# Performance work log

Measured on AMD Instinct MI355X. Metric: run time of the kernel, lower is better.

## Reference

```python
import jax, jax.numpy as jnp
import numpy as np

NUM_EXPERT = 8
IN_FEAT = 1024
OUT_FEAT = 1024
N_TOKENS = 8192


def setup_inputs() -> dict:
    key = jax.random.key(0)
    k_inp, k_gate, k_w = jax.random.split(key, 3)
    inp = jax.random.normal(k_inp, (N_TOKENS, IN_FEAT), dtype=jnp.float32)
    gate = jax.random.randint(k_gate, (N_TOKENS,), 0, NUM_EXPERT, dtype=jnp.int32)
    # FMoELinear weight: [num_expert, out_feat, in_feat], kaiming-uniform-like init
    bound = 1.0 / np.sqrt(IN_FEAT)
    weight = jax.random.uniform(
        k_w, (NUM_EXPERT, OUT_FEAT, IN_FEAT), dtype=jnp.float32,
        minval=-bound, maxval=bound)
    return {"inp": inp, "gate": gate, "weight": weight}


def reference(inp, gate, weight):
    # out[i] = weight[gate[i]] @ inp[i]  (top-1 MoE dispatch + grouped GEMM + combine)
    # Loop over the small fixed expert set via scan; each step does a masked
    # dense GEMM so only tokens routed to expert e contribute.
    n, _ = inp.shape
    num_expert, out_feat, _ = weight.shape

    def body(acc, ew):
        e, w_e = ew  # w_e: [out_feat, in_feat]
        mask = (gate == e).astype(inp.dtype)[:, None]  # [n, 1]
        acc = acc + (inp * mask) @ w_e.T               # [n, out_feat]
        return acc, None

    init = jnp.zeros((n, out_feat), dtype=inp.dtype)
    out, _ = jax.lax.scan(body, init, (jnp.arange(num_expert), weight))
    return out
```

## Files before the change

kernel.cpp:

```cpp
#include <hip/hip_runtime.h>
#include <hip/hip_bf16.h>

#define N_TOKENS 8192
#define IN_FEAT 1024
#define OUT_FEAT 1024
#define NUM_EXPERT 8

#define BM 128
#define BN 128
#define BK 32

typedef __bf16 bf16x8 __attribute__((ext_vector_type(8)));
typedef float f32x4 __attribute__((ext_vector_type(4)));

__device__ __forceinline__ unsigned int rne16(float x) {
    union { float f; unsigned int u; } c;
    c.f = x;
    unsigned int u = c.u;
    u += 0x7fffu + ((u >> 16) & 1u);
    return u >> 16;
}
__device__ __forceinline__ unsigned int pk2(float x, float y) {
    return rne16(x) | (rne16(y) << 16);
}

__device__ __forceinline__ void load_lds16(const void* g, void* l) {
    __builtin_amdgcn_global_load_lds(
        (const __attribute__((address_space(1))) unsigned int*)g,
        (__attribute__((address_space(3))) unsigned int*)l,
        16, 0, 0);
}

__global__ __launch_bounds__(1024) void moe_setup(const int* __restrict__ gate,
                                                  int* __restrict__ seg,
                                                  int* __restrict__ cur) {
    __shared__ int lc[NUM_EXPERT];
    const int t = threadIdx.x;
    const int lane = t & 63;
    if (t < NUM_EXPERT) lc[t] = 0;
    __syncthreads();
    #pragma unroll
    for (int i = 0; i < 8; ++i) {
        int g = gate[t + i * 1024];
        #pragma unroll
        for (int e = 0; e < NUM_EXPERT; ++e) {
            unsigned long long m = __ballot(g == e);
            if (lane == 0 && m) atomicAdd(&lc[e], __popcll(m));
        }
    }
    __syncthreads();
    if (t == 0) {
        int s = 0;
        #pragma unroll
        for (int e = 0; e < NUM_EXPERT; ++e) { seg[e] = s; cur[e] = s; s += lc[e]; }
        seg[NUM_EXPERT] = s;
    }
}

__global__ __launch_bounds__(256) void moe_scatter(const int* __restrict__ gate,
                                                   int* __restrict__ cur,
                                                   int* __restrict__ perm) {
    const int t = threadIdx.x;
    const int lane = t & 63;
    const unsigned long long lt = (lane == 0) ? 0ull : (~0ull >> (64 - lane));
    const int i = blockIdx.x * 256 + t;
    int g = gate[i];
    #pragma unroll
    for (int e = 0; e < NUM_EXPERT; ++e) {
        unsigned long long m = __ballot(g == e);
        if (g == e) {
            int rank = __popcll(m & lt);
            int leader = (int)__ffsll((unsigned long long)m) - 1;
            int p0 = 0;
            if (rank == 0) p0 = atomicAdd(&cur[e], __popcll(m));
            p0 = __shfl(p0, leader);
            perm[p0 + rank] = i;
        }
    }
}

__global__ __launch_bounds__(256) void moe_prep(const float* __restrict__ inp,
                                                const float* __restrict__ weight,
                                                const int* __restrict__ perm,
                                                unsigned int* __restrict__ A2,
                                                unsigned int* __restrict__ W2) {
    const int bid = blockIdx.x;
    const int t = threadIdx.x;
    const int wave = t >> 6, lane = t & 63;
    const float* src;
    unsigned int* dst;
    if (bid < 2048) {
        int row = bid * 4 + wave;
        src = inp + perm[row] * IN_FEAT;
        dst = A2 + row * (IN_FEAT / 2);
    } else {
        int row = (bid - 2048) * 4 + wave;
        src = weight + row * IN_FEAT;
        dst = W2 + row * (IN_FEAT / 2);
    }
    #pragma unroll
    for (int ps = 0; ps < 2; ++ps) {
        float4 v0 = *(const float4*)(src + ps * 512 + lane * 8);
        float4 v1 = *(const float4*)(src + ps * 512 + lane * 8 + 4);
        uint4 o;
        o.x = pk2(v0.x, v0.y); o.y = pk2(v0.z, v0.w);
        o.z = pk2(v1.x, v1.y); o.w = pk2(v1.z, v1.w);
        *(uint4*)(dst + ps * 256 + lane * 4) = o;
    }
}

__global__ __launch_bounds__(256, 4) void moe_gemm(
    const unsigned short* __restrict__ A2,
    const unsigned short* __restrict__ W2,
    const int* __restrict__ perm,
    const int* __restrict__ seg,
    float* __restrict__ out) {

    const int bid = blockIdx.x;
    const int e = bid & 7;
    const int ntile = (bid >> 3) & 7;
    const int mtile = bid >> 6;

    const int base = seg[e];
    const int cnt = seg[e + 1] - base;
    if (mtile * BM >= cnt) return;
    const int tbase = base + mtile * BM;
    int rows = cnt - mtile * BM; if (rows > BM) rows = BM;

    __shared__ __align__(16) unsigned short lA[2][BM * BK];
    __shared__ __align__(16) unsigned short lB[2][BN * BK];

    const int t = threadIdx.x;

    const int crow = t >> 2;
    const int p = (t & 3) ^ (crow & 3);
    int ar0 = tbase + crow;       if (ar0 > N_TOKENS - 1) ar0 = N_TOKENS - 1;
    int ar1 = tbase + 64 + crow;  if (ar1 > N_TOKENS - 1) ar1 = N_TOKENS - 1;
    const unsigned short* gA0 = A2 + ar0 * IN_FEAT + p * 8;
    const unsigned short* gA1 = A2 + ar1 * IN_FEAT + p * 8;
    const unsigned short* gB0 = W2 + e * (OUT_FEAT * IN_FEAT)
                                + (ntile * BN + crow) * IN_FEAT + p * 8;
    const unsigned short* gB1 = gB0 + 64 * IN_FEAT;
    const int dofs = t * 8;
    const int dofs2 = (t + 256) * 8;

    const int wave = t >> 6;
    const int lane = t & 63;
    const int wm = (wave & 1) << 6;
    const int wn = (wave >> 1) << 6;
    const int l15 = lane & 15;
    const int quad = lane >> 4;
    const int qx = quad ^ (l15 & 3);
    const int fofsA = (wm + l15) * BK + qx * 8;
    const int fofsB = (wn + l15) * BK + qx * 8;

    f32x4 acc[4][4];
    #pragma unroll
    for (int i = 0; i < 4; ++i)
        #pragma unroll
        for (int j = 0; j < 4; ++j)
            acc[i][j] = (f32x4)0.0f;

    load_lds16(gA0, &lA[0][dofs]);
    load_lds16(gA1, &lA[0][dofs2]);
    load_lds16(gB0, &lB[0][dofs]);
    load_lds16(gB1, &lB[0][dofs2]);

    #pragma unroll 1
    for (int kk = 0; kk < 16; ++kk) {
        const int k0 = kk * 64;

        __syncthreads();
        load_lds16(gA0 + k0 + 32, &lA[1][dofs]);
        load_lds16(gA1 + k0 + 32, &lA[1][dofs2]);
        load_lds16(gB0 + k0 + 32, &lB[1][dofs]);
        load_lds16(gB1 + k0 + 32, &lB[1][dofs2]);

        {
            bf16x8 af[4], bq[4];
            #pragma unroll
            for (int i = 0; i < 4; ++i)
                af[i] = *(const bf16x8*)&lA[0][fofsA + i * 16 * BK];
            #pragma unroll
            for (int j = 0; j < 4; ++j)
                bq[j] = *(const bf16x8*)&lB[0][fofsB + j * 16 * BK];
            #pragma unroll
            for (int i = 0; i < 4; ++i)
                #pragma unroll
                for (int j = 0; j < 4; ++j)
                    acc[i][j] = __builtin_amdgcn_mfma_f32_16x16x32_bf16(
                        af[i], bq[j], acc[i][j], 0, 0, 0);
        }

        __syncthreads();
        if (kk < 15) {
            load_lds16(gA0 + k0 + 64, &lA[0][dofs]);
            load_lds16(gA1 + k0 + 64, &lA[0][dofs2]);
            load_lds16(gB0 + k0 + 64, &lB[0][dofs]);
            load_lds16(gB1 + k0 + 64, &lB[0][dofs2]);
        }

        {
            bf16x8 af[4], bq[4];
            #pragma unroll
            for (int i = 0; i < 4; ++i)
                af[i] = *(const bf16x8*)&lA[1][fofsA + i * 16 * BK];
            #pragma unroll
            for (int j = 0; j < 4; ++j)
                bq[j] = *(const bf16x8*)&lB[1][fofsB + j * 16 * BK];
            #pragma unroll
            for (int i = 0; i < 4; ++i)
                #pragma unroll
                for (int j = 0; j < 4; ++j)
                    acc[i][j] = __builtin_amdgcn_mfma_f32_16x16x32_bf16(
                        af[i], bq[j], acc[i][j], 0, 0, 0);
        }
    }

    #pragma unroll
    for (int mi = 0; mi < 4; ++mi) {
        #pragma unroll
        for (int r = 0; r < 4; ++r) {
            int row = wm + mi * 16 + quad * 4 + r;
            if (row < rows) {
                int token = perm[tbase + row];
                float* op = out + token * OUT_FEAT + ntile * BN + wn;
                #pragma unroll
                for (int ni = 0; ni < 4; ++ni)
                    op[ni * 16 + l15] = acc[mi][ni][r];
            }
        }
    }
}

#define FLDSW 20
__global__ __launch_bounds__(256, 4) void moe_gemm_fb(
    const float* __restrict__ inp,
    const float* __restrict__ weight,
    const int* __restrict__ perm,
    const int* __restrict__ seg,
    float* __restrict__ out) {

    const int bid = blockIdx.x;
    const int mtile = bid >> 7;
    const int e = (bid >> 4) & 7;
    const int ntile = bid & 15;

    const int base = seg[e];
    const int cnt = seg[e + 1] - base;
    if (mtile * 128 >= cnt) return;

    __shared__ unsigned int lA[128 * FLDSW];
    __shared__ unsigned int lB[64 * FLDSW];
    __shared__ int rowids[128];

    const int t = threadIdx.x;
    if (t < 128) {
        int r = mtile * 128 + t;
        rowids[t] = (r < cnt) ? perm[base + r] : -1;
    }
    __syncthreads();

    const int srow = t >> 1;
    const int scol = (t & 1) << 4;
    const int tokA = rowids[srow];
    const bool aval = (tokA >= 0);
    const float* aptr = inp + (aval ? tokA : 0) * IN_FEAT + scol;
    const int sdstA = srow * FLDSW + (scol >> 1);
    const int browB = t >> 2;
    const int bcol = (t & 3) << 3;
    const float* bptr = weight + e * (OUT_FEAT * IN_FEAT)
                        + (ntile * 64 + browB) * IN_FEAT + bcol;
    const int sdstB = browB * FLDSW + (bcol >> 1);

    const int wave = t >> 6;
    const int lane = t & 63;
    const int wm = (wave & 1) << 6;
    const int wn = (wave >> 1) << 5;
    const int l15 = lane & 15;
    const int quad = lane >> 4;

    f32x4 acc[4][2];
    #pragma unroll
    for (int i = 0; i < 4; ++i)
        #pragma unroll
        for (int j = 0; j < 2; ++j)
            acc[i][j] = (f32x4)0.0f;

    float4 ra[4], rb[2];
    {
        const float4* ap = (const float4*)aptr;
        const float4* bp = (const float4*)bptr;
        #pragma unroll
        for (int i = 0; i < 4; ++i) ra[i] = ap[i];
        #pragma unroll
        for (int i = 0; i < 2; ++i) rb[i] = bp[i];
    }

    for (int k0 = 0; k0 < IN_FEAT; k0 += 32) {
        unsigned int ua[8], ub[4];
        #pragma unroll
        for (int i = 0; i < 4; ++i) {
            ua[2 * i]     = pk2(ra[i].x, ra[i].y);
            ua[2 * i + 1] = pk2(ra[i].z, ra[i].w);
        }
        #pragma unroll
        for (int i = 0; i < 2; ++i) {
            ub[2 * i]     = pk2(rb[i].x, rb[i].y);
            ub[2 * i + 1] = pk2(rb[i].z, rb[i].w);
        }
        if (!aval) {
            #pragma unroll
            for (int i = 0; i < 8; ++i) ua[i] = 0u;
        }

        __syncthreads();
        *(uint4*)&lA[sdstA]     = make_uint4(ua[0], ua[1], ua[2], ua[3]);
        *(uint4*)&lA[sdstA + 4] = make_uint4(ua[4], ua[5], ua[6], ua[7]);
        *(uint4*)&lB[sdstB]     = make_uint4(ub[0], ub[1], ub[2], ub[3]);
        __syncthreads();

        if (k0 + 32 < IN_FEAT) {
            const float4* ap = (const float4*)(aptr + k0 + 32);
            const float4* bp = (const float4*)(bptr + k0 + 32);
            #pragma unroll
            for (int i = 0; i < 4; ++i) ra[i] = ap[i];
            #pragma unroll
            for (int i = 0; i < 2; ++i) rb[i] = bp[i];
        }

        bf16x8 af[4], bq[2];
        #pragma unroll
        for (int i = 0; i < 4; ++i)
            af[i] = *(const bf16x8*)&lA[(wm + i * 16 + l15) * FLDSW + (quad << 2)];
        #pragma unroll
        for (int j = 0; j < 2; ++j)
            bq[j] = *(const bf16x8*)&lB[(wn + j * 16 + l15) * FLDSW + (quad << 2)];

        #pragma unroll
        for (int i = 0; i < 4; ++i)
            #pragma unroll
            for (int j = 0; j < 2; ++j)
                acc[i][j] = __builtin_amdgcn_mfma_f32_16x16x32_bf16(
                    af[i], bq[j], acc[i][j], 0, 0, 0);
    }

    #pragma unroll
    for (int mi = 0; mi < 4; ++mi) {
        #pragma unroll
        for (int r = 0; r < 4; ++r) {
            int row = wm + mi * 16 + quad * 4 + r;
            int token = rowids[row];
            if (token >= 0) {
                float* op = out + token * OUT_FEAT + ntile * 64 + wn;
                #pragma unroll
                for (int ni = 0; ni < 2; ++ni)
                    op[ni * 16 + l15] = acc[mi][ni][r];
            }
        }
    }
}

extern "C" void kernel_launch(void* const* d_in, const int* in_sizes, int n_in,
                              void* d_out, int out_size, void* d_ws, size_t ws_size,
                              hipStream_t stream) {
    const float* inp = (const float*)d_in[0];
    const int* gate = (const int*)d_in[1];
    const float* weight = (const float*)d_in[2];
    float* out = (float*)d_out;

    int* perm = (int*)d_ws;
    int* seg = perm + N_TOKENS;
    int* cur = seg + 16;

    const size_t need = 65536 + 2ull * N_TOKENS * IN_FEAT * 2;
    const int useBf16 = (ws_size >= need);
    unsigned int* A2 = (unsigned int*)((char*)d_ws + 65536);
    unsigned int* W2 = A2 + (N_TOKENS * IN_FEAT / 2);

    moe_setup<<<1, 1024, 0, stream>>>(gate, seg, cur);
    moe_scatter<<<N_TOKENS / 256, 256, 0, stream>>>(gate, cur, perm);

    if (useBf16) {
        moe_prep<<<4096, 256, 0, stream>>>(inp, weight, perm, A2, W2);
        moe_gemm<<<4096, 256, 0, stream>>>((const unsigned short*)A2,
                                           (const unsigned short*)W2,
                                           perm, seg, out);
    } else {
        moe_gemm_fb<<<8192, 256, 0, stream>>>(inp, weight, perm, seg, out);
    }
}
```

Measured before the change: 157.1 us.

## Merge routing kernels and use two-wave GEMM blocks with 64x128 warp tiles

Fuses the expert-count and scatter kernels into one single-block sort kernel that keeps the gate values in registers and the cursors in shared memory, removing one launch and the global cursor atomics. The GEMM block drops from 256 to 128 threads, so each wave now computes a 64x128 output tile with 32 accumulators instead of 16. This doubles the B-fragment reuse per LDS read but raises register pressure and halves the waves available per block to hide latency. The scatter now runs inside a single workgroup, so its ordering work is serialized there.

```diff
diff --git a/kernel.cpp b/kernel.cpp
--- a/kernel.cpp
+++ b/kernel.cpp
@@ -31,20 +31,27 @@
         16, 0, 0);
 }
 
-__global__ __launch_bounds__(1024) void moe_setup(const int* __restrict__ gate,
-                                                  int* __restrict__ seg,
-                                                  int* __restrict__ cur) {
+__global__ __launch_bounds__(1024) void moe_sort(const int* __restrict__ gate,
+                                                 int* __restrict__ seg,
+                                                 int* __restrict__ perm) {
     __shared__ int lc[NUM_EXPERT];
+    __shared__ int cur[NUM_EXPERT];
     const int t = threadIdx.x;
     const int lane = t & 63;
+    const unsigned long long lt = (lane == 0) ? 0ull : (~0ull >> (64 - lane));
+
     if (t < NUM_EXPERT) lc[t] = 0;
     __syncthreads();
+
+    int gv[8];
+    #pragma unroll
+    for (int i = 0; i < 8; ++i) gv[i] = gate[t + i * 1024];
+
     #pragma unroll
     for (int i = 0; i < 8; ++i) {
-        int g = gate[t + i * 1024];
         #pragma unroll
         for (int e = 0; e < NUM_EXPERT; ++e) {
-            unsigned long long m = __ballot(g == e);
+            unsigned long long m = __ballot(gv[i] == e);
             if (lane == 0 && m) atomicAdd(&lc[e], __popcll(m));
         }
     }
@@ -55,26 +62,23 @@
         for (int e = 0; e < NUM_EXPERT; ++e) { seg[e] = s; cur[e] = s; s += lc[e]; }
         seg[NUM_EXPERT] = s;
     }
-}
-
-__global__ __launch_bounds__(256) void moe_scatter(const int* __restrict__ gate,
-                                                   int* __restrict__ cur,
-                                                   int* __restrict__ perm) {
-    const int t = threadIdx.x;
-    const int lane = t & 63;
-    const unsigned long long lt = (lane == 0) ? 0ull : (~0ull >> (64 - lane));
-    const int i = blockIdx.x * 256 + t;
-    int g = gate[i];
-    #pragma unroll
-    for (int e = 0; e < NUM_EXPERT; ++e) {
-        unsigned long long m = __ballot(g == e);
-        if (g == e) {
-            int rank = __popcll(m & lt);
-            int leader = (int)__ffsll((unsigned long long)m) - 1;
-            int p0 = 0;
-            if (rank == 0) p0 = atomicAdd(&cur[e], __popcll(m));
-            p0 = __shfl(p0, leader);
-            perm[p0 + rank] = i;
+    __syncthreads();
+
+    #pragma unroll
+    for (int i = 0; i < 8; ++i) {
+        const int g = gv[i];
+        const int idx = t + i * 1024;
+        #pragma unroll
+        for (int e = 0; e < NUM_EXPERT; ++e) {
+            unsigned long long m = __ballot(g == e);
+            if (g == e) {
+                int rank = __popcll(m & lt);
+                int leader = (int)__ffsll((unsigned long long)m) - 1;
+                int p0 = 0;
+                if (rank == 0) p0 = atomicAdd(&cur[e], __popcll(m));
+                p0 = __shfl(p0, leader);
+                perm[p0 + rank] = idx;
+            }
         }
     }
 }
@@ -109,7 +113,7 @@
     }
 }
 
-__global__ __launch_bounds__(256, 4) void moe_gemm(
+__global__ __launch_bounds__(128, 2) void moe_gemm(
     const unsigned short* __restrict__ A2,
     const unsigned short* __restrict__ W2,
     const int* __restrict__ perm,
@@ -131,102 +135,87 @@
     __shared__ __align__(16) unsigned short lB[2][BN * BK];
 
     const int t = threadIdx.x;
-
-    const int crow = t >> 2;
-    const int p = (t & 3) ^ (crow & 3);
-    int ar0 = tbase + crow;       if (ar0 > N_TOKENS - 1) ar0 = N_TOKENS - 1;
-    int ar1 = tbase + 64 + crow;  if (ar1 > N_TOKENS - 1) ar1 = N_TOKENS - 1;
-    const unsigned short* gA0 = A2 + ar0 * IN_FEAT + p * 8;
-    const unsigned short* gA1 = A2 + ar1 * IN_FEAT + p * 8;
-    const unsigned short* gB0 = W2 + e * (OUT_FEAT * IN_FEAT)
-                                + (ntile * BN + crow) * IN_FEAT + p * 8;
-    const unsigned short* gB1 = gB0 + 64 * IN_FEAT;
-    const int dofs = t * 8;
-    const int dofs2 = (t + 256) * 8;
-
     const int wave = t >> 6;
     const int lane = t & 63;
-    const int wm = (wave & 1) << 6;
-    const int wn = (wave >> 1) << 6;
+
+    const unsigned short* srcA[4];
+    const unsigned short* srcB[4];
+    int ldsOfs[4];
+    #pragma unroll
+    for (int j = 0; j < 4; ++j) {
+        const int c = j * 128 + t;
+        const int r = c >> 2;
+        const int p = (c & 3) ^ (r & 3);
+        int ar = tbase + r; if (ar > N_TOKENS - 1) ar = N_TOKENS - 1;
+        srcA[j] = A2 + ar * IN_FEAT + p * 8;
+        srcB[j] = W2 + e * (OUT_FEAT * IN_FEAT) + (ntile * BN + r) * IN_FEAT + p * 8;
+        ldsOfs[j] = c * 8;
+    }
+
     const int l15 = lane & 15;
     const int quad = lane >> 4;
     const int qx = quad ^ (l15 & 3);
-    const int fofsA = (wm + l15) * BK + qx * 8;
-    const int fofsB = (wn + l15) * BK + qx * 8;
-
-    f32x4 acc[4][4];
+    const int fofsA = (wave * 64 + l15) * BK + qx * 8;
+    const int fofsB = l15 * BK + qx * 8;
+
+    f32x4 acc[4][8];
     #pragma unroll
     for (int i = 0; i < 4; ++i)
         #pragma unroll
-        for (int j = 0; j < 4; ++j)
+        for (int j = 0; j < 8; ++j)
             acc[i][j] = (f32x4)0.0f;
 
-    load_lds16(gA0, &lA[0][dofs]);
-    load_lds16(gA1, &lA[0][dofs2]);
-    load_lds16(gB0, &lB[0][dofs]);
-    load_lds16(gB1, &lB[0][dofs2]);
+#define ISSUE(buf, kofs) do {                                          \
+        _Pragma("unroll")                                              \
+        for (int j = 0; j < 4; ++j) {                                  \
+            load_lds16(srcA[j] + (kofs), &lA[buf][ldsOfs[j]]);         \
+            load_lds16(srcB[j] + (kofs), &lB[buf][ldsOfs[j]]);         \
+        }                                                              \
+    } while (0)
+
+#define COMPUTE(buf) do {                                              \
+        bf16x8 af[4], bq[8];                                           \
+        _Pragma("unroll")                                              \
+        for (int i = 0; i < 4; ++i)                                    \
+            af[i] = *(const bf16x8*)&lA[buf][fofsA + i * 16 * BK];     \
+        _Pragma("unroll")                                              \
+        for (int j = 0; j < 8; ++j)                                    \
+            bq[j] = *(const bf16x8*)&lB[buf][fofsB + j * 16 * BK];     \
+        _Pragma("unroll")                                              \
+        for (int i = 0; i < 4; ++i)                                    \
+            _Pragma("unroll")                                          \
+            for (int j = 0; j < 8; ++j)                                \
+                acc[i][j] = __builtin_amdgcn_mfma_f32_16x16x32_bf16(   \
+                    af[i], bq[j], acc[i][j], 0, 0, 0);                 \
+    } while (0)
+
+    ISSUE(0, 0);
 
     #pragma unroll 1
     for (int kk = 0; kk < 16; ++kk) {
         const int k0 = kk * 64;
 
         __syncthreads();
-        load_lds16(gA0 + k0 + 32, &lA[1][dofs]);
-        load_lds16(gA1 + k0 + 32, &lA[1][dofs2]);
-        load_lds16(gB0 + k0 + 32, &lB[1][dofs]);
-        load_lds16(gB1 + k0 + 32, &lB[1][dofs2]);
-
-        {
-            bf16x8 af[4], bq[4];
-            #pragma unroll
-            for (int i = 0; i < 4; ++i)
-                af[i] = *(const bf16x8*)&lA[0][fofsA + i * 16 * BK];
-            #pragma unroll
-            for (int j = 0; j < 4; ++j)
-                bq[j] = *(const bf16x8*)&lB[0][fofsB + j * 16 * BK];
-            #pragma unroll
-            for (int i = 0; i < 4; ++i)
-                #pragma unroll
-                for (int j = 0; j < 4; ++j)
-                    acc[i][j] = __builtin_amdgcn_mfma_f32_16x16x32_bf16(
-                        af[i], bq[j], acc[i][j], 0, 0, 0);
-        }
+        ISSUE(1, k0 + 32);
+        COMPUTE(0);
 
         __syncthreads();
-        if (kk < 15) {
-            load_lds16(gA0 + k0 + 64, &lA[0][dofs]);
-            load_lds16(gA1 + k0 + 64, &lA[0][dofs2]);
-            load_lds16(gB0 + k0 + 64, &lB[0][dofs]);
-            load_lds16(gB1 + k0 + 64, &lB[0][dofs2]);
-        }
-
-        {
-            bf16x8 af[4], bq[4];
-            #pragma unroll
-            for (int i = 0; i < 4; ++i)
-                af[i] = *(const bf16x8*)&lA[1][fofsA + i * 16 * BK];
-            #pragma unroll
-            for (int j = 0; j < 4; ++j)
-                bq[j] = *(const bf16x8*)&lB[1][fofsB + j * 16 * BK];
-            #pragma unroll
-            for (int i = 0; i < 4; ++i)
-                #pragma unroll
-                for (int j = 0; j < 4; ++j)
-                    acc[i][j] = __builtin_amdgcn_mfma_f32_16x16x32_bf16(
-                        af[i], bq[j], acc[i][j], 0, 0, 0);
-        }
-    }
+        if (kk < 15) ISSUE(0, k0 + 64);
+        COMPUTE(1);
+    }
+#undef COMPUTE
+#undef ISSUE
 
     #pragma unroll
     for (int mi = 0; mi < 4; ++mi) {
         #pragma unroll
         for (int r = 0; r < 4; ++r) {
-            int row = wm + mi * 16 + quad * 4 + r;
+            int row = wave * 64 + mi * 16 + quad * 4 + r;
             if (row < rows) {
                 int token = perm[tbase + row];
-                float* op = out + token * OUT_FEAT + ntile * BN + wn;
+                float* op = out + token * OUT_FEAT + ntile * BN;
                 #pragma unroll
-                for (int ni = 0; ni < 4; ++ni)
+                for (int ni = 0; ni < 8; ++ni)
                     op[ni * 16 + l15] = acc[mi][ni][r];
             }
         }
@@ -371,19 +360,17 @@
 
     int* perm = (int*)d_ws;
     int* seg = perm + N_TOKENS;
-    int* cur = seg + 16;
 
     const size_t need = 65536 + 2ull * N_TOKENS * IN_FEAT * 2;
     const int useBf16 = (ws_size >= need);
     unsigned int* A2 = (unsigned int*)((char*)d_ws + 65536);
     unsigned int* W2 = A2 + (N_TOKENS * IN_FEAT / 2);
 
-    moe_setup<<<1, 1024, 0, stream>>>(gate, seg, cur);
-    moe_scatter<<<N_TOKENS / 256, 256, 0, stream>>>(gate, cur, perm);
+    moe_sort<<<1, 1024, 0, stream>>>(gate, seg, perm);
 
     if (useBf16) {
         moe_prep<<<4096, 256, 0, stream>>>(inp, weight, perm, A2, W2);
-        moe_gemm<<<4096, 256, 0, stream>>>((const unsigned short*)A2,
+        moe_gemm<<<4096, 128, 0, stream>>>((const unsigned short*)A2,
                                            (const unsigned short*)W2,
                                            perm, seg, out);
     } else {
```

Result: slower. 160.5 us (+2.2%).
